# Kernel tuning notes

Measured on AMD Instinct MI355X. Metric: run time of the kernel, lower is better.

Reference implementation:

```python
import jax, jax.numpy as jnp
import numpy as np

NUM_HEADS = 4

def setup_inputs() -> dict:
    key = jax.random.key(0)
    ks = jax.random.split(key, 5)
    B, H, W, C = 4, 64, 64, 256
    x = jax.random.normal(ks[0], (B, H, W, C), dtype=jnp.float32)
    w_qkv = jax.random.normal(ks[1], (C, 3 * C), dtype=jnp.float32) * (C ** -0.5)
    b_qkv = jax.random.normal(ks[2], (3 * C,), dtype=jnp.float32) * 0.02
    w_out = jax.random.normal(ks[3], (C, C), dtype=jnp.float32) * (C ** -0.5)
    b_out = jax.random.normal(ks[4], (C,), dtype=jnp.float32) * 0.02
    return {"x": x, "w_qkv": w_qkv, "b_qkv": b_qkv, "w_out": w_out, "b_out": b_out}

def reference(x, w_qkv, b_qkv, w_out, b_out):
    B, H, W, C = x.shape
    nh = NUM_HEADS
    hd = C // nh
    scale = hd ** -0.5
    N = H * W
    # qkv projection: [B, N, 3, nh, hd]
    qkv = (x.reshape(B, N, C) @ w_qkv + b_qkv).reshape(B, N, 3, nh, hd)
    q, k, v = jnp.moveaxis(qkv, 2, 0)          # each [B, N, nh, hd]
    q = jnp.swapaxes(q, 1, 2)                  # [B, nh, N, hd]
    k = jnp.swapaxes(k, 1, 2)
    v = jnp.swapaxes(v, 1, 2)
    attn = jax.nn.softmax(jnp.einsum('bhnd,bhmd->bhnm', q * scale, k), axis=-1)
    o = jnp.einsum('bhnm,bhmd->bhnd', attn, v)  # [B, nh, N, hd]
    o = jnp.swapaxes(o, 1, 2).reshape(B, H, W, C)
    return o @ w_out + b_out
```

## Files before the change

kernel.cpp:

```cpp
#include <hip/hip_runtime.h>
#include <stdint.h>

typedef unsigned short u16;
typedef __attribute__((ext_vector_type(8))) short bf16x8;
typedef __attribute__((ext_vector_type(4))) float f32x4;
typedef __attribute__((ext_vector_type(16))) float f32x16;

#define QSCL 0.1803368801111244f

#define GLD_LDS16(g, l) __builtin_amdgcn_global_load_lds( \
    (const __attribute__((address_space(1))) void*)(g),    \
    (__attribute__((address_space(3))) void*)(l), 16, 0, 0)

#if __has_builtin(__builtin_amdgcn_exp2f)
#define EXP2(x) __builtin_amdgcn_exp2f(x)
#else
#define EXP2(x) __builtin_exp2f(x)
#endif

__device__ __forceinline__ u16 f2bf(float f) {
    union { uint32_t i; float f; } v; v.f = f;
    uint32_t i = v.i;
    return (u16)((i + 0x7FFFu + ((i >> 16) & 1u)) >> 16);
}

__device__ __forceinline__ void p32swap(uint32_t& a, uint32_t& b) {
#if __has_builtin(__builtin_amdgcn_permlane32_swap)
    auto r = __builtin_amdgcn_permlane32_swap(a, b, false, false);
    a = (uint32_t)r[0]; b = (uint32_t)r[1];
#else
    const int hh = (int)((threadIdx.x & 63) >> 5);
    uint32_t ta = (uint32_t)__shfl_xor((int)a, 32);
    uint32_t tb = (uint32_t)__shfl_xor((int)b, 32);
    uint32_t na = hh ? tb : a;
    uint32_t nb = hh ? b : ta;
    a = na; b = nb;
#endif
}

__device__ __forceinline__ bf16x8 mk8(uint32_t a, uint32_t b, uint32_t c, uint32_t d) {
    union { uint32_t u[4]; bf16x8 v; } x;
    x.u[0] = a; x.u[1] = b; x.u[2] = c; x.u[3] = d;
    return x.v;
}

__global__ __launch_bounds__(256)
void transpose_kernel(const float* __restrict__ src, u16* __restrict__ dst,
                      int R, int Ctiles) {
    __shared__ u16 T[64][68];
    const int t = threadIdx.x;
    const int rt = blockIdx.x / Ctiles;
    const int ct = blockIdx.x % Ctiles;
    const int C = Ctiles << 6;

    for (int i = 0; i < 4; i++) {
        int idx = t + 256 * i;
        int row = idx >> 4;
        int col4 = (idx & 15) << 2;
        float4 d = *(const float4*)(src + (size_t)(rt * 64 + row) * C + ct * 64 + col4);
        T[col4 + 0][row] = f2bf(d.x);
        T[col4 + 1][row] = f2bf(d.y);
        T[col4 + 2][row] = f2bf(d.z);
        T[col4 + 3][row] = f2bf(d.w);
    }
    __syncthreads();
    for (int i = 0; i < 4; i++) {
        int idx = t + 256 * i;
        int row = idx >> 4;
        int col4 = (idx & 15) << 2;
        uint2 d = *(const uint2*)&T[row][col4];
        *(uint2*)(dst + (size_t)(ct * 64 + row) * R + rt * 64 + col4) = d;
    }
}

__global__ __launch_bounds__(256)
void convert_kernel(const float* __restrict__ x, u16* __restrict__ xbf) {
    size_t i = ((size_t)blockIdx.x * 256 + threadIdx.x) * 4;
    float4 d = *(const float4*)(x + i);
    u16 e[4] = {f2bf(d.x), f2bf(d.y), f2bf(d.z), f2bf(d.w)};
    *(uint2*)(xbf + i) = *(uint2*)e;
}

__global__ __launch_bounds__(256)
void gemm_qkv_old(const float* __restrict__ X, const u16* __restrict__ Wt,
                  const float* __restrict__ Bias, u16* __restrict__ QK,
                  u16* __restrict__ Vt) {
    __shared__ __align__(16) u16 As[64][40];
    __shared__ __align__(16) u16 Bts[64][40];

    const int t = threadIdx.x;
    const int lane = t & 63;
    const int wave = t >> 6;
    const int l15 = lane & 15;
    const int l4 = lane >> 4;

    const int ntile = blockIdx.x % 12;
    const int mbase = (blockIdx.x / 12) << 6;

    f32x4 acc[4];
    for (int c = 0; c < 4; c++) acc[c] = (f32x4){0.f, 0.f, 0.f, 0.f};

    for (int kc = 0; kc < 256; kc += 32) {
        __syncthreads();
        for (int i = 0; i < 2; i++) {
            int idx = t + 256 * i;
            int row = idx >> 3;
            int col4 = (idx & 7) << 2;
            float4 d = *(const float4*)(X + (size_t)(mbase + row) * 256 + kc + col4);
            u16 e[4] = {f2bf(d.x), f2bf(d.y), f2bf(d.z), f2bf(d.w)};
            *(uint2*)&As[row][col4] = *(uint2*)e;
        }
        for (int i = 0; i < 2; i++) {
            int idx = t + 256 * i;
            int row = idx >> 3;
            int col4 = (idx & 7) << 2;
            uint2 w = *(const uint2*)(Wt + (size_t)(ntile * 64 + row) * 256 + kc + col4);
            *(uint2*)&Bts[row][col4] = w;
        }
        __syncthreads();

        bf16x8 a = *(const bf16x8*)&As[wave * 16 + l15][l4 * 8];
        for (int c = 0; c < 4; c++) {
            bf16x8 b = *(const bf16x8*)&Bts[c * 16 + l15][l4 * 8];
            acc[c] = __builtin_amdgcn_mfma_f32_16x16x32_bf16(a, b, acc[c], 0, 0, 0);
        }
    }

    if (ntile < 8) {
        const float scl = (ntile < 4) ? QSCL : 1.0f;
        for (int c = 0; c < 4; c++) {
            int colc = c * 16 + l15;
            float bv = Bias[ntile * 64 + colc];
            for (int r = 0; r < 4; r++) {
                int row = mbase + wave * 16 + l4 * 4 + r;
                QK[(size_t)row * 512 + ntile * 64 + colc] = f2bf((acc[c][r] + bv) * scl);
            }
        }
    } else {
        const int h = ntile - 8;
        for (int c = 0; c < 4; c++) {
            int d = c * 16 + l15;
            float bv = Bias[512 + h * 64 + d];
            int n = mbase + wave * 16 + l4 * 4;
            int b = n >> 12;
            int nin = n & 4095;
            u16 e[4] = {f2bf(acc[c][0] + bv), f2bf(acc[c][1] + bv),
                        f2bf(acc[c][2] + bv), f2bf(acc[c][3] + bv)};
            *(uint2*)(Vt + ((size_t)(b * 4 + h) * 64 + d) * 4096 + nin) = *(uint2*)e;
        }
    }
}

__global__ __launch_bounds__(256)
void gemm_out_old(const u16* __restrict__ Wt2, const float* __restrict__ Bias,
                  float* __restrict__ IO) {
    __shared__ __align__(16) u16 As[64][264];
    __shared__ __align__(16) u16 Wts[256][40];

    const int t = threadIdx.x;
    const int lane = t & 63;
    const int wave = t >> 6;
    const int l15 = lane & 15;
    const int l4 = lane >> 4;
    const int mbase = blockIdx.x << 6;

    for (int i = 0; i < 16; i++) {
        int idx = t + 256 * i;
        int row = idx >> 6;
        int col4 = (idx & 63) << 2;
        float4 d = *(const float4*)(IO + (size_t)(mbase + row) * 256 + col4);
        u16 e[4] = {f2bf(d.x), f2bf(d.y), f2bf(d.z), f2bf(d.w)};
        *(uint2*)&As[row][col4] = *(uint2*)e;
    }

    f32x4 acc[4][4];
    for (int nt = 0; nt < 4; nt++)
        for (int c = 0; c < 4; c++) acc[nt][c] = (f32x4){0.f, 0.f, 0.f, 0.f};

    for (int kc = 0; kc < 256; kc += 32) {
        __syncthreads();
        for (int i = 0; i < 8; i++) {
            int idx = t + 256 * i;
            int row = idx >> 3;
            int col4 = (idx & 7) << 2;
            uint2 w = *(const uint2*)(Wt2 + (size_t)row * 256 + kc + col4);
            *(uint2*)&Wts[row][col4] = w;
        }
        __syncthreads();

        bf16x8 a = *(const bf16x8*)&As[wave * 16 + l15][kc + l4 * 8];
        for (int nt = 0; nt < 4; nt++)
            for (int c = 0; c < 4; c++) {
                bf16x8 b = *(const bf16x8*)&Wts[nt * 64 + c * 16 + l15][l4 * 8];
                acc[nt][c] = __builtin_amdgcn_mfma_f32_16x16x32_bf16(a, b, acc[nt][c], 0, 0, 0);
            }
    }

    for (int nt = 0; nt < 4; nt++)
        for (int c = 0; c < 4; c++) {
            int coln = nt * 64 + c * 16 + l15;
            float bv = Bias[coln];
            for (int r = 0; r < 4; r++) {
                int row = mbase + wave * 16 + l4 * 4 + r;
                IO[(size_t)row * 256 + coln] = acc[nt][c][r] + bv;
            }
        }
}

__global__ __launch_bounds__(256)
void gemm_qkv_new(const u16* __restrict__ Abf, const u16* __restrict__ Bt,
                  const float* __restrict__ Bias, u16* __restrict__ QK,
                  u16* __restrict__ Vt) {
    __shared__ __align__(16) u16 As[128 * 32];
    __shared__ __align__(16) u16 Bs[128 * 32];

    const int t = threadIdx.x;
    const int lane = t & 63;
    const int wave = t >> 6;
    const int l15 = lane & 15;
    const int l4 = lane >> 4;
    const int wm = wave >> 1, wn = wave & 1;

    const int mb = blockIdx.x / 6;
    const int nb = blockIdx.x % 6;

    const u16* gA[2]; const u16* gB[2]; int ldsoff[2];
    #pragma unroll
    for (int i = 0; i < 2; i++) {
        int chunk = i * 256 + t;
        int row = chunk >> 2;
        int sch = (chunk & 3) ^ (row & 3);
        gA[i] = Abf + (size_t)(mb * 128 + row) * 256 + sch * 8;
        gB[i] = Bt + (size_t)(nb * 128 + row) * 256 + sch * 8;
        ldsoff[i] = (i * 256 + wave * 64) * 8;
    }
    int offA[4], offB[4];
    #pragma unroll
    for (int c = 0; c < 4; c++) {
        offA[c] = (wm * 64 + c * 16 + l15) * 32 + ((l4 ^ (l15 & 3)) * 8);
        offB[c] = (wn * 64 + c * 16 + l15) * 32 + ((l4 ^ (l15 & 3)) * 8);
    }

    f32x4 acc[4][4];
    #pragma unroll
    for (int cm = 0; cm < 4; cm++)
        for (int cn = 0; cn < 4; cn++) acc[cm][cn] = (f32x4){0.f, 0.f, 0.f, 0.f};

    for (int kc = 0; kc < 256; kc += 32) {
        __syncthreads();
        #pragma unroll
        for (int i = 0; i < 2; i++) {
            GLD_LDS16(gA[i] + kc, As + ldsoff[i]);
            GLD_LDS16(gB[i] + kc, Bs + ldsoff[i]);
        }
        __syncthreads();

        bf16x8 a[4], b[4];
        #pragma unroll
        for (int c = 0; c < 4; c++) {
            a[c] = *(const bf16x8*)(As + offA[c]);
            b[c] = *(const bf16x8*)(Bs + offB[c]);
        }
        #pragma unroll
        for (int cm = 0; cm < 4; cm++)
            #pragma unroll
            for (int cn = 0; cn < 4; cn++)
                acc[cm][cn] = __builtin_amdgcn_mfma_f32_16x16x32_bf16(
                    a[cm], b[cn], acc[cm][cn], 0, 0, 0);
    }

    #pragma unroll
    for (int cn = 0; cn < 4; cn++) {
        int n = nb * 128 + wn * 64 + cn * 16 + l15;
        float bv = Bias[n];
        int slice = n >> 6;
        if (slice < 4) {
            #pragma unroll
            for (int cm = 0; cm < 4; cm++) {
                int m0 = mb * 128 + wm * 64 + cm * 16 + l4 * 4;
                for (int r = 0; r < 4; r++)
                    QK[(size_t)(m0 + r) * 512 + n] = f2bf((acc[cm][cn][r] + bv) * QSCL);
            }
        } else if (slice < 8) {
            #pragma unroll
            for (int cm = 0; cm < 4; cm++) {
                int m0 = mb * 128 + wm * 64 + cm * 16 + l4 * 4;
                for (int r = 0; r < 4; r++)
                    QK[(size_t)(m0 + r) * 512 + n] = f2bf(acc[cm][cn][r] + bv);
            }
        } else {
            int h = slice - 8;
            int d = n & 63;
            #pragma unroll
            for (int cm = 0; cm < 4; cm++) {
                int m0 = mb * 128 + wm * 64 + cm * 16 + l4 * 4;
                int b_ = m0 >> 12;
                int nin = m0 & 4095;
                u16 e[4] = {f2bf(acc[cm][cn][0] + bv), f2bf(acc[cm][cn][1] + bv),
                            f2bf(acc[cm][cn][2] + bv), f2bf(acc[cm][cn][3] + bv)};
                *(uint2*)(Vt + ((size_t)(b_ * 4 + h) * 64 + d) * 4096 + nin) = *(uint2*)e;
            }
        }
    }
}

__global__ __launch_bounds__(256)
void gemm_out_new(const u16* __restrict__ Obf, const u16* __restrict__ Wt2,
                  const float* __restrict__ Bias, float* __restrict__ out) {
    __shared__ __align__(16) u16 As[128 * 32];
    __shared__ __align__(16) u16 Bs[128 * 32];

    const int t = threadIdx.x;
    const int lane = t & 63;
    const int wave = t >> 6;
    const int l15 = lane & 15;
    const int l4 = lane >> 4;
    const int wm = wave >> 1, wn = wave & 1;

    const int mb = blockIdx.x >> 1;
    const int nb = blockIdx.x & 1;

    const u16* gA[2]; const u16* gB[2]; int ldsoff[2];
    #pragma unroll
    for (int i = 0; i < 2; i++) {
        int chunk = i * 256 + t;
        int row = chunk >> 2;
        int sch = (chunk & 3) ^ (row & 3);
        gA[i] = Obf + (size_t)(mb * 128 + row) * 256 + sch * 8;
        gB[i] = Wt2 + (size_t)(nb * 128 + row) * 256 + sch * 8;
        ldsoff[i] = (i * 256 + wave * 64) * 8;
    }
    int offA[4], offB[4];
    #pragma unroll
    for (int c = 0; c < 4; c++) {
        offA[c] = (wm * 64 + c * 16 + l15) * 32 + ((l4 ^ (l15 & 3)) * 8);
        offB[c] = (wn * 64 + c * 16 + l15) * 32 + ((l4 ^ (l15 & 3)) * 8);
    }

    f32x4 acc[4][4];
    #pragma unroll
    for (int cm = 0; cm < 4; cm++)
        for (int cn = 0; cn < 4; cn++) acc[cm][cn] = (f32x4){0.f, 0.f, 0.f, 0.f};

    for (int kc = 0; kc < 256; kc += 32) {
        __syncthreads();
        #pragma unroll
        for (int i = 0; i < 2; i++) {
            GLD_LDS16(gA[i] + kc, As + ldsoff[i]);
            GLD_LDS16(gB[i] + kc, Bs + ldsoff[i]);
        }
        __syncthreads();

        bf16x8 a[4], b[4];
        #pragma unroll
        for (int c = 0; c < 4; c++) {
            a[c] = *(const bf16x8*)(As + offA[c]);
            b[c] = *(const bf16x8*)(Bs + offB[c]);
        }
        #pragma unroll
        for (int cm = 0; cm < 4; cm++)
            #pragma unroll
            for (int cn = 0; cn < 4; cn++)
                acc[cm][cn] = __builtin_amdgcn_mfma_f32_16x16x32_bf16(
                    a[cm], b[cn], acc[cm][cn], 0, 0, 0);
    }

    #pragma unroll
    for (int cn = 0; cn < 4; cn++) {
        int n = nb * 128 + wn * 64 + cn * 16 + l15;
        float bv = Bias[n];
        #pragma unroll
        for (int cm = 0; cm < 4; cm++) {
            int m0 = mb * 128 + wm * 64 + cm * 16 + l4 * 4;
            for (int r = 0; r < 4; r++)
                out[(size_t)(m0 + r) * 256 + n] = acc[cm][cn][r] + bv;
        }
    }
}

__global__ __launch_bounds__(256, 4)
void attn_kernel(const u16* __restrict__ QK, const u16* __restrict__ Vt,
                 float* __restrict__ Of, u16* __restrict__ Obf, int writebf,
                 int bhmask, int bhbits) {
    __shared__ __align__(16) u16 Kt[2][64][64];
    __shared__ __align__(16) u16 Vts[2][64][64];

    const int t = threadIdx.x;
    const int lane = t & 63;
    const int wave = t >> 6;
    const int l31 = lane & 31;
    const int h = lane >> 5;
    const int jw = wave & 1;
    const int qw = wave >> 1;

    const int bh = blockIdx.x & bhmask;
    const int qb = blockIdx.x >> bhbits;
    const int b = bh >> 2;
    const int hd = bh & 3;

    const size_t qkbase = (size_t)b * 4096 * 512;
    const size_t vtbase = (size_t)bh * 64 * 4096;
    const int q = qb * 64 + qw * 32 + l31;

    const u16* gk[2]; const u16* gv[2]; u16* lk[2]; u16* lv[2];
    #pragma unroll
    for (int i = 0; i < 2; i++) {
        int ck = i * 256 + t;
        int row = ck >> 3;
        int sch = (ck & 7) ^ (row & 7);
        gk[i] = QK + qkbase + (size_t)row * 512 + 256 + hd * 64 + sch * 8;
        gv[i] = Vt + vtbase + (size_t)row * 4096 + sch * 8;
        lk[i] = &Kt[0][0][0] + (i * 256 + wave * 64) * 8;
        lv[i] = &Vts[0][0][0] + (i * 256 + wave * 64) * 8;
    }

    int kfo[4];
    {
        int row = jw * 32 + l31;
        int sw = row & 7;
        #pragma unroll
        for (int dc = 0; dc < 4; dc++)
            kfo[dc] = row * 64 + ((dc * 2 + h) ^ sw) * 8;
    }
    int vfo[2][2];
    #pragma unroll
    for (int dh = 0; dh < 2; dh++) {
        int row = dh * 32 + l31;
        int sw = row & 7;
        #pragma unroll
        for (int J = 0; J < 2; J++)
            vfo[dh][J] = row * 64 + ((jw * 4 + J * 2 + h) ^ sw) * 8;
    }

    bf16x8 qf[4];
    #pragma unroll
    for (int dc = 0; dc < 4; dc++)
        qf[dc] = *(const bf16x8*)(QK + qkbase + (size_t)q * 512
                                  + hd * 64 + dc * 16 + h * 8);

    const f32x16 z16 = {0.f, 0.f, 0.f, 0.f, 0.f, 0.f, 0.f, 0.f,
                        0.f, 0.f, 0.f, 0.f, 0.f, 0.f, 0.f, 0.f};
    f32x16 Oacc[2];
    Oacc[0] = z16; Oacc[1] = z16;
    float lsum = 0.f;

    auto stageKV = [&](int buf, int jn) {
        #pragma unroll
        for (int i = 0; i < 2; i++) {
            GLD_LDS16(gk[i] + (size_t)jn * 32768, lk[i] + buf * 4096);
            GLD_LDS16(gv[i] + jn * 64,            lv[i] + buf * 4096);
        }
    };

    auto body = [&](int par, int jn) {
        __syncthreads();
        stageKV(par ^ 1, jn);

        const u16* kb = &Kt[0][0][0] + par * 4096;
        const u16* vb = &Vts[0][0][0] + par * 4096;

        bf16x8 kf0 = *(const bf16x8*)(kb + kfo[0]);
        bf16x8 kf1 = *(const bf16x8*)(kb + kfo[1]);
        bf16x8 kf2 = *(const bf16x8*)(kb + kfo[2]);
        bf16x8 kf3 = *(const bf16x8*)(kb + kfo[3]);

        f32x16 s;
        s = __builtin_amdgcn_mfma_f32_32x32x16_bf16(kf0, qf[0], z16, 0, 0, 0);
        s = __builtin_amdgcn_mfma_f32_32x32x16_bf16(kf1, qf[1], s, 0, 0, 0);
        s = __builtin_amdgcn_mfma_f32_32x32x16_bf16(kf2, qf[2], s, 0, 0, 0);
        s = __builtin_amdgcn_mfma_f32_32x32x16_bf16(kf3, qf[3], s, 0, 0, 0);

        bf16x8 vf00 = *(const bf16x8*)(vb + vfo[0][0]);
        bf16x8 vf01 = *(const bf16x8*)(vb + vfo[0][1]);
        bf16x8 vf10 = *(const bf16x8*)(vb + vfo[1][0]);
        bf16x8 vf11 = *(const bf16x8*)(vb + vfo[1][1]);

        uint32_t w[8];
        float ls = 0.f;
        #pragma unroll
        for (int k = 0; k < 8; k++) {
            float p0 = EXP2(s[2 * k]);
            float p1 = EXP2(s[2 * k + 1]);
            ls += p0 + p1;
            asm("v_cvt_pk_bf16_f32 %0, %1, %2" : "=v"(w[k]) : "v"(p0), "v"(p1));
        }
        lsum += ls;

        p32swap(w[0], w[2]); p32swap(w[1], w[3]);
        p32swap(w[4], w[6]); p32swap(w[5], w[7]);

        bf16x8 bp0 = mk8(w[0], w[1], w[2], w[3]);
        bf16x8 bp1 = mk8(w[4], w[5], w[6], w[7]);

        Oacc[0] = __builtin_amdgcn_mfma_f32_32x32x16_bf16(vf00, bp0, Oacc[0], 0, 0, 0);
        Oacc[0] = __builtin_amdgcn_mfma_f32_32x32x16_bf16(vf01, bp1, Oacc[0], 0, 0, 0);
        Oacc[1] = __builtin_amdgcn_mfma_f32_32x32x16_bf16(vf10, bp0, Oacc[1], 0, 0, 0);
        Oacc[1] = __builtin_amdgcn_mfma_f32_32x32x16_bf16(vf11, bp1, Oacc[1], 0, 0, 0);
    };

    stageKV(0, 0);
    for (int jt = 0; jt < 64; jt += 2) {
        body(0, jt + 1);
        body(1, (jt + 2) & 63);
    }

    lsum += __shfl_xor(lsum, 32);

    __syncthreads();
    float* sc  = (float*)&Kt[0][0][0];
    float* scl = (float*)&Vts[0][0][0];
    const int swl = lane & 7;

    if (jw) {
        float* ob = sc + qw * 2048 + lane * 32;
        #pragma unroll
        for (int dh = 0; dh < 2; dh++)
            #pragma unroll
            for (int i = 0; i < 4; i++) {
                int k8 = dh * 4 + i;
                f32x4 c = {Oacc[dh][4 * i + 0], Oacc[dh][4 * i + 1],
                           Oacc[dh][4 * i + 2], Oacc[dh][4 * i + 3]};
                *(f32x4*)(ob + ((k8 ^ swl) * 4)) = c;
            }
        scl[qw * 64 + lane] = lsum;
    }
    __syncthreads();
    if (!jw) {
        float* ob = sc + qw * 2048 + lane * 32;
        float lt = lsum + scl[qw * 64 + lane];
        float inv = 1.f / lt;
        size_t row = (size_t)b * 4096 + q;
        #pragma unroll
        for (int dh = 0; dh < 2; dh++)
            #pragma unroll
            for (int i = 0; i < 4; i++) {
                int k8 = dh * 4 + i;
                f32x4 pR = *(f32x4*)(ob + ((k8 ^ swl) * 4));
                f32x4 o;
                #pragma unroll
                for (int r = 0; r < 4; r++)
                    o[r] = (Oacc[dh][4 * i + r] + pR[r]) * inv;
                int col = hd * 64 + dh * 32 + i * 8 + h * 4;
                if (writebf) {
                    u16 e[4] = {f2bf(o[0]), f2bf(o[1]), f2bf(o[2]), f2bf(o[3])};
                    *(uint2*)(Obf + row * 256 + col) = *(uint2*)e;
                } else {
                    *(f32x4*)(Of + row * 256 + col) = o;
                }
            }
    }
}

extern "C" void kernel_launch(void* const* d_in, const int* in_sizes, int n_in,
                              void* d_out, int out_size, void* d_ws, size_t ws_size,
                              hipStream_t stream) {
    const float* x     = (const float*)d_in[0];
    const float* w_qkv = (const float*)d_in[1];
    const float* b_qkv = (const float*)d_in[2];
    const float* w_out = (const float*)d_in[3];
    const float* b_out = (const float*)d_in[4];
    float* out = (float*)d_out;

    char* ws = (char*)d_ws;
    u16* Wt  = (u16*)ws;
    u16* Wt2 = (u16*)(ws + 393216);
    u16* QK  = (u16*)(ws + 524288);
    u16* Vt  = (u16*)(ws + 524288 + 16777216);
    u16* XO  = (u16*)(ws + 524288 + 16777216 + 8388608);
    const size_t NEED_NEW = 524288 + 16777216 + 8388608 + 8388608;

    transpose_kernel<<<dim3(48), dim3(256), 0, stream>>>(w_qkv, Wt, 256, 12);
    transpose_kernel<<<dim3(16), dim3(256), 0, stream>>>(w_out, Wt2, 256, 4);

    if (ws_size >= NEED_NEW) {
        convert_kernel<<<dim3(4096), dim3(256), 0, stream>>>(x, XO);
        gemm_qkv_new<<<dim3(768), dim3(256), 0, stream>>>(XO, Wt, b_qkv, QK, Vt);
        attn_kernel<<<dim3(1024), dim3(256), 0, stream>>>(
            QK, Vt, out, XO, 1, 15, 4);
        gemm_out_new<<<dim3(256), dim3(256), 0, stream>>>(XO, Wt2, b_out, out);
    } else {
        gemm_qkv_old<<<dim3(3072), dim3(256), 0, stream>>>(x, Wt, b_qkv, QK, Vt);
        attn_kernel<<<dim3(1024), dim3(256), 0, stream>>>(
            QK, Vt, out, (u16*)nullptr, 0, 15, 4);
        gemm_out_old<<<dim3(256), dim3(256), 0, stream>>>(Wt2, b_out, out);
    }
}
```

Before: 189.1 us.

## Fuse prep kernels, compute softmax row sums via MFMA, add MFMA priority hints

Merges the two weight transposes and the x-to-bf16 conversion into one prep launch, removing two kernel launches. In the attention inner loop, the scalar VALU accumulation of exp values for the softmax denominator is replaced by two extra MFMAs against a ones matrix, moving that work onto the matrix cores. This also removes the final cross-half shuffle. s_setprio is raised around the MFMA groups to favour matrix-issue scheduling. The extra MFMAs add matrix-core load and accumulator registers, and the row sum now comes from bf16-rounded probabilities.

```diff
diff --git a/kernel.cpp b/kernel.cpp
--- a/kernel.cpp
+++ b/kernel.cpp
@@ -44,13 +44,13 @@
     return x.v;
 }
 
-__global__ __launch_bounds__(256)
-void transpose_kernel(const float* __restrict__ src, u16* __restrict__ dst,
-                      int R, int Ctiles) {
+__device__ __forceinline__ void transpose_body(const float* __restrict__ src,
+                                               u16* __restrict__ dst,
+                                               int R, int Ctiles, int bid) {
     __shared__ u16 T[64][68];
     const int t = threadIdx.x;
-    const int rt = blockIdx.x / Ctiles;
-    const int ct = blockIdx.x % Ctiles;
+    const int rt = bid / Ctiles;
+    const int ct = bid % Ctiles;
     const int C = Ctiles << 6;
 
     for (int i = 0; i < 4; i++) {
@@ -74,11 +74,26 @@
 }
 
 __global__ __launch_bounds__(256)
-void convert_kernel(const float* __restrict__ x, u16* __restrict__ xbf) {
-    size_t i = ((size_t)blockIdx.x * 256 + threadIdx.x) * 4;
-    float4 d = *(const float4*)(x + i);
-    u16 e[4] = {f2bf(d.x), f2bf(d.y), f2bf(d.z), f2bf(d.w)};
-    *(uint2*)(xbf + i) = *(uint2*)e;
+void transpose_kernel(const float* __restrict__ src, u16* __restrict__ dst,
+                      int R, int Ctiles) {
+    transpose_body(src, dst, R, Ctiles, blockIdx.x);
+}
+
+__global__ __launch_bounds__(256)
+void prep_kernel(const float* __restrict__ w_qkv, u16* __restrict__ Wt,
+                 const float* __restrict__ w_out, u16* __restrict__ Wt2,
+                 const float* __restrict__ x, u16* __restrict__ xbf) {
+    const int bid = blockIdx.x;
+    if (bid < 48) {
+        transpose_body(w_qkv, Wt, 256, 12, bid);
+    } else if (bid < 64) {
+        transpose_body(w_out, Wt2, 256, 4, bid - 48);
+    } else {
+        size_t i = ((size_t)(bid - 64) * 256 + threadIdx.x) * 4;
+        float4 d = *(const float4*)(x + i);
+        u16 e[4] = {f2bf(d.x), f2bf(d.y), f2bf(d.z), f2bf(d.w)};
+        *(uint2*)(xbf + i) = *(uint2*)e;
+    }
 }
 
 __global__ __launch_bounds__(256)
@@ -438,11 +453,13 @@
         qf[dc] = *(const bf16x8*)(QK + qkbase + (size_t)q * 512
                                   + hd * 64 + dc * 16 + h * 8);
 
+    const bf16x8 onesf = mk8(0x3F803F80u, 0x3F803F80u, 0x3F803F80u, 0x3F803F80u);
+
     const f32x16 z16 = {0.f, 0.f, 0.f, 0.f, 0.f, 0.f, 0.f, 0.f,
                         0.f, 0.f, 0.f, 0.f, 0.f, 0.f, 0.f, 0.f};
     f32x16 Oacc[2];
     Oacc[0] = z16; Oacc[1] = z16;
-    float lsum = 0.f;
+    f32x16 lacc = z16;
 
     auto stageKV = [&](int buf, int jn) {
         #pragma unroll
@@ -464,11 +481,13 @@
         bf16x8 kf2 = *(const bf16x8*)(kb + kfo[2]);
         bf16x8 kf3 = *(const bf16x8*)(kb + kfo[3]);
 
+        __builtin_amdgcn_s_setprio(1);
         f32x16 s;
         s = __builtin_amdgcn_mfma_f32_32x32x16_bf16(kf0, qf[0], z16, 0, 0, 0);
         s = __builtin_amdgcn_mfma_f32_32x32x16_bf16(kf1, qf[1], s, 0, 0, 0);
         s = __builtin_amdgcn_mfma_f32_32x32x16_bf16(kf2, qf[2], s, 0, 0, 0);
         s = __builtin_amdgcn_mfma_f32_32x32x16_bf16(kf3, qf[3], s, 0, 0, 0);
+        __builtin_amdgcn_s_setprio(0);
 
         bf16x8 vf00 = *(const bf16x8*)(vb + vfo[0][0]);
         bf16x8 vf01 = *(const bf16x8*)(vb + vfo[0][1]);
@@ -476,15 +495,12 @@
         bf16x8 vf11 = *(const bf16x8*)(vb + vfo[1][1]);
 
         uint32_t w[8];
-        float ls = 0.f;
         #pragma unroll
         for (int k = 0; k < 8; k++) {
             float p0 = EXP2(s[2 * k]);
             float p1 = EXP2(s[2 * k + 1]);
-            ls += p0 + p1;
             asm("v_cvt_pk_bf16_f32 %0, %1, %2" : "=v"(w[k]) : "v"(p0), "v"(p1));
         }
-        lsum += ls;
 
         p32swap(w[0], w[2]); p32swap(w[1], w[3]);
         p32swap(w[4], w[6]); p32swap(w[5], w[7]);
@@ -492,10 +508,14 @@
         bf16x8 bp0 = mk8(w[0], w[1], w[2], w[3]);
         bf16x8 bp1 = mk8(w[4], w[5], w[6], w[7]);
 
+        __builtin_amdgcn_s_setprio(1);
         Oacc[0] = __builtin_amdgcn_mfma_f32_32x32x16_bf16(vf00, bp0, Oacc[0], 0, 0, 0);
         Oacc[0] = __builtin_amdgcn_mfma_f32_32x32x16_bf16(vf01, bp1, Oacc[0], 0, 0, 0);
         Oacc[1] = __builtin_amdgcn_mfma_f32_32x32x16_bf16(vf10, bp0, Oacc[1], 0, 0, 0);
         Oacc[1] = __builtin_amdgcn_mfma_f32_32x32x16_bf16(vf11, bp1, Oacc[1], 0, 0, 0);
+        lacc    = __builtin_amdgcn_mfma_f32_32x32x16_bf16(onesf, bp0, lacc, 0, 0, 0);
+        lacc    = __builtin_amdgcn_mfma_f32_32x32x16_bf16(onesf, bp1, lacc, 0, 0, 0);
+        __builtin_amdgcn_s_setprio(0);
     };
 
     stageKV(0, 0);
@@ -504,7 +524,7 @@
         body(1, (jt + 2) & 63);
     }
 
-    lsum += __shfl_xor(lsum, 32);
+    float lsum = lacc[0];
 
     __syncthreads();
     float* sc  = (float*)&Kt[0][0][0];
@@ -569,16 +589,15 @@
     u16* XO  = (u16*)(ws + 524288 + 16777216 + 8388608);
     const size_t NEED_NEW = 524288 + 16777216 + 8388608 + 8388608;
 
-    transpose_kernel<<<dim3(48), dim3(256), 0, stream>>>(w_qkv, Wt, 256, 12);
-    transpose_kernel<<<dim3(16), dim3(256), 0, stream>>>(w_out, Wt2, 256, 4);
-
     if (ws_size >= NEED_NEW) {
-        convert_kernel<<<dim3(4096), dim3(256), 0, stream>>>(x, XO);
+        prep_kernel<<<dim3(4160), dim3(256), 0, stream>>>(w_qkv, Wt, w_out, Wt2, x, XO);
         gemm_qkv_new<<<dim3(768), dim3(256), 0, stream>>>(XO, Wt, b_qkv, QK, Vt);
         attn_kernel<<<dim3(1024), dim3(256), 0, stream>>>(
             QK, Vt, out, XO, 1, 15, 4);
         gemm_out_new<<<dim3(256), dim3(256), 0, stream>>>(XO, Wt2, b_out, out);
     } else {
+        transpose_kernel<<<dim3(48), dim3(256), 0, stream>>>(w_qkv, Wt, 256, 12);
+        transpose_kernel<<<dim3(16), dim3(256), 0, stream>>>(w_out, Wt2, 256, 4);
         gemm_qkv_old<<<dim3(3072), dim3(256), 0, stream>>>(x, Wt, b_qkv, QK, Vt);
         attn_kernel<<<dim3(1024), dim3(256), 0, stream>>>(
             QK, Vt, out, (u16*)nullptr, 0, 15, 4);
```

New measurement: 197.4 us. 1.04x slower.
